# Kernel tuning notes

Hardware: AMD Instinct MI355X
Metric: run time of the kernel (lower is better)

## Reference

```python
import jax, jax.numpy as jnp
import numpy as np

B, D, H, W = 16, 384, 64, 64
Dq, Dv, NH, DFF = 768, 384, 12, 1536
EPS = 1e-5


def setup_inputs() -> dict:
    key = jax.random.key(0)
    ks = jax.random.split(key, 8)

    def w(k, out_c, in_c):
        return (jax.random.normal(k, (out_c, in_c), jnp.float32) / np.float32(np.sqrt(in_c)))

    return {
        "x": jax.random.normal(ks[0], (B, D, H, W), jnp.float32),
        "ln1_w": jnp.ones((D, H, W), jnp.float32),
        "ln1_b": jnp.zeros((D, H, W), jnp.float32),
        "qw": w(ks[1], Dq, D), "qb": jnp.zeros((Dq,), jnp.float32),
        "kw": w(ks[2], Dq, D), "kb": jnp.zeros((Dq,), jnp.float32),
        "vw": w(ks[3], Dv, D), "vb": jnp.zeros((Dv,), jnp.float32),
        "hu_w": w(ks[4], D, Dv), "hu_b": jnp.zeros((D,), jnp.float32),
        "ln2_w": jnp.ones((D, H, W), jnp.float32),
        "ln2_b": jnp.zeros((D, H, W), jnp.float32),
        "ff1_w": w(ks[5], DFF, D), "ff1_b": jnp.zeros((DFF,), jnp.float32),
        "ff2_w": w(ks[6], D, DFF), "ff2_b": jnp.zeros((D,), jnp.float32),
    }


def layernorm(x, w, b):
    # torch.nn.LayerNorm((D, H, W)): normalize over last 3 dims, biased var
    mu = x.mean(axis=(1, 2, 3), keepdims=True)
    var = x.var(axis=(1, 2, 3), keepdims=True)
    return (x - mu) * jax.lax.rsqrt(var + EPS) * w + b


def conv1x1(x, w, b):
    # 1x1 conv == channel-mixing matmul; x: (B, Cin, H, W), w: (Cout, Cin)
    return jnp.einsum('bdhw,od->bohw', x, w) + b[None, :, None, None]


def reference(x, ln1_w, ln1_b, qw, qb, kw, kb, vw, vb, hu_w, hu_b,
              ln2_w, ln2_b, ff1_w, ff1_b, ff2_w, ff2_b):
    a = layernorm(x, ln1_w, ln1_b)
    Q = conv1x1(a, qw, qb)  # (B, Dq, H, W)
    K = conv1x1(a, kw, kb)  # (B, Dq, H, W)
    V = conv1x1(a, vw, vb)  # (B, Dv, H, W)

    Q = jax.nn.softmax(Q, axis=1)  # softmax over channels (subtract-max is built in)
    K = jax.nn.softmax(K.reshape(B, Dq, H * W), axis=-1).reshape(B, Dq, H, W)

    Qh = Q.reshape(B, NH, Dq // NH, H, W)
    Kh = K.reshape(B, NH, Dq // NH, H, W)
    Vh = V.reshape(B, NH, Dv // NH, H, W)

    # kernel_size=1: adaptive_avg_pool2d(KV, 1) * 1 == spatial mean of K (x) V,
    # and the grouped 1x1 conv is a per-(batch,head) (Dv/h x Dq/h) matmul on Q.
    KV = jnp.einsum('bhqyx,bhvyx->bhqv', Kh, Vh) / np.float32(H * W)
    QKV = jnp.einsum('bhqv,bhqyx->bhvyx', KV, Qh).reshape(B, Dv, H, W)

    attn = conv1x1(QKV, hu_w, hu_b)  # head unification, (B, D, H, W)
    x = x + attn
    x = layernorm(x, ln2_w, ln2_b)
    ff = conv1x1(jax.nn.gelu(conv1x1(x, ff1_w, ff1_b), approximate=False), ff2_w, ff2_b)
    return x + ff
```

## Files before the change

kernel.cpp:

```cpp
#include <hip/hip_runtime.h>
#include <hip/hip_bf16.h>

using u16 = unsigned short;
typedef __attribute__((ext_vector_type(4))) float f32x4;
typedef __bf16 bf16x8 __attribute__((ext_vector_type(8)));
typedef short s16x4 __attribute__((ext_vector_type(4)));
typedef short s16x8 __attribute__((ext_vector_type(8)));

#define DEVI __device__ __forceinline__

DEVI float b2f(u16 u) {
    union { unsigned i; float f; } x; x.i = ((unsigned)u) << 16; return x.f;
}
DEVI u16 f2b(float f) {
    union { float f; unsigned i; } x; x.f = f;
    unsigned r = (x.i + 0x7fffu + ((x.i >> 16) & 1u)) >> 16;
    return (u16)r;
}

DEVI float gelu_fast(float v) {
    float t = v * (1.5957691f + 0.0713548162f * v * v);
    return v / (1.f + __expf(-t));
}

static constexpr long long PX = 1572864LL;
static constexpr long long PQ = 3145728LL;
static constexpr long long PH = 6291456LL;

DEVI void gl_lds16(const u16* g, u16* l) {
    __builtin_amdgcn_global_load_lds(
        (const __attribute__((address_space(1))) unsigned int*)g,
        (__attribute__((address_space(3))) unsigned int*)l, 16, 0, 0);
}

__global__ __launch_bounds__(256)
void wconv_kernel(const float* __restrict__ qw, const float* __restrict__ kw,
                  const float* __restrict__ vw, const float* __restrict__ huw,
                  const float* __restrict__ ff1w, const float* __restrict__ ff2w,
                  u16* __restrict__ wcv)
{
    int blk = blockIdx.x;
    const float* src; u16* dst; int lb;
    if      (blk < 288)  { src = qw;   dst = wcv;           lb = blk; }
    else if (blk < 576)  { src = kw;   dst = wcv + 294912;  lb = blk - 288; }
    else if (blk < 720)  { src = vw;   dst = wcv + 589824;  lb = blk - 576; }
    else if (blk < 864)  { src = huw;  dst = wcv + 737280;  lb = blk - 720; }
    else if (blk < 1440) { src = ff1w; dst = wcv + 884736;  lb = blk - 864; }
    else                 { src = ff2w; dst = wcv + 1474560; lb = blk - 1440; }
    int i = (lb * 256 + threadIdx.x) * 4;
    f32x4 v = *(const f32x4*)(src + i);
    s16x4 o;
#pragma unroll
    for (int j = 0; j < 4; ++j) o[j] = (short)f2b(v[j]);
    *(s16x4*)(dst + i) = o;
}

__global__ __launch_bounds__(256)
void bcat_kernel(const float* __restrict__ qb, const float* __restrict__ kb,
                 const float* __restrict__ vb, float* __restrict__ o)
{
    int i = blockIdx.x * 256 + threadIdx.x;
    if (i < 768)       o[i] = qb[i];
    else if (i < 1536) o[i] = kb[i - 768];
    else if (i < 1920) o[i] = vb[i - 1536];
}

__global__ __launch_bounds__(256, 4)
void gemm_qkv_kernel(const u16* __restrict__ A, long long strideA,
                     const u16* __restrict__ Bw,
                     const float* __restrict__ bias,
                     u16* __restrict__ Q, u16* __restrict__ Kd, u16* __restrict__ V,
                     int K)
{
    const int tid = threadIdx.x;
    const int lane = tid & 63;
    const int wv = tid >> 6;
    const int wr = wv >> 1, wc = wv & 1;
    const int l15 = lane & 15, l4 = lane >> 4;
    const int bm = blockIdx.x, bn = blockIdx.y, bz = blockIdx.z;

    A += (long long)bz * strideA;
    u16* dstBase; int Nout; int colBase;
    if (bn < 6)       { dstBase = Q  + (long long)bz * PQ; Nout = 768; colBase = bn * 128; }
    else if (bn < 12) { dstBase = Kd + (long long)bz * PQ; Nout = 768; colBase = (bn - 6) * 128; }
    else              { dstBase = V  + (long long)bz * PX; Nout = 384; colBase = (bn - 12) * 128; }

    __shared__ u16 lds[2][128 * 64];

    f32x4 acc[4][4] = {};

    auto stage = [&](int kt) {
#pragma unroll
        for (int i = 0; i < 4; ++i) {
            int cid = tid + i * 256;
            int row = cid >> 3, c8 = cid & 7;
            int c8s = c8 ^ (row & 7);
            gl_lds16(A + (long long)(bm * 128 + row) * K + kt + c8s * 8,
                     &lds[0][cid * 8]);
        }
#pragma unroll
        for (int i = 0; i < 4; ++i) {
            int cid = tid + i * 256;
            int row = cid >> 3, c8 = cid & 7;
            int c8s = c8 ^ (row & 7);
            gl_lds16(Bw + (long long)(bn * 128 + row) * K + kt + c8s * 8,
                     &lds[1][cid * 8]);
        }
    };

    auto compute = [&]() {
#pragma unroll
        for (int kk = 0; kk < 2; ++kk) {
            bf16x8 af[4], bfr[4];
#pragma unroll
            for (int mi = 0; mi < 4; ++mi) {
                int row = wr * 64 + mi * 16 + l15;
                int idx8 = (kk * 4 + l4) ^ (row & 7);
                af[mi] = *(const bf16x8*)&lds[0][row * 64 + idx8 * 8];
            }
#pragma unroll
            for (int ni = 0; ni < 4; ++ni) {
                int row = wc * 64 + ni * 16 + l15;
                int idx8 = (kk * 4 + l4) ^ (row & 7);
                bfr[ni] = *(const bf16x8*)&lds[1][row * 64 + idx8 * 8];
            }
#pragma unroll
            for (int mi = 0; mi < 4; ++mi)
#pragma unroll
                for (int ni = 0; ni < 4; ++ni)
                    acc[mi][ni] = __builtin_amdgcn_mfma_f32_16x16x32_bf16(af[mi], bfr[ni], acc[mi][ni], 0, 0, 0);
        }
    };

    stage(0);
    asm volatile("s_waitcnt vmcnt(0)" ::: "memory");
    __syncthreads();
    for (int kt = 64; kt < K; kt += 64) {
        compute();
        __syncthreads();
        stage(kt);
        asm volatile("s_waitcnt vmcnt(0)" ::: "memory");
        __syncthreads();
    }
    compute();

    u16* st = &lds[0][0];
#pragma unroll
    for (int p = 0; p < 2; ++p) {
        __syncthreads();
        if (wr == p) {
#pragma unroll
            for (int ni = 0; ni < 4; ++ni) {
                int colL = wc * 64 + ni * 16 + l15;
                float bv = bias[bn * 128 + colL];
#pragma unroll
                for (int mi = 0; mi < 4; ++mi) {
#pragma unroll
                    for (int r = 0; r < 4; ++r)
                        st[(mi * 16 + l4 * 4 + r) * 136 + colL] = f2b(acc[mi][ni][r] + bv);
                }
            }
        }
        __syncthreads();
        int lr = tid >> 2, q = tid & 3;
        const u16* src = st + lr * 136 + q * 32;
        u16* dst = dstBase + (long long)(bm * 128 + p * 64 + lr) * Nout + colBase + q * 32;
#pragma unroll
        for (int j = 0; j < 4; ++j)
            *(s16x8*)(dst + j * 8) = *(const s16x8*)(src + j * 8);
    }
}

__global__ __launch_bounds__(256, 4)
void gemm_attn_kernel(const u16* __restrict__ A, long long strideA,
                      const u16* __restrict__ Bw, long long strideB,
                      const float* __restrict__ bias,
                      const float* __restrict__ x,
                      u16* __restrict__ sT,
                      float* __restrict__ part2, int K)
{
    const int tid = threadIdx.x;
    const int lane = tid & 63;
    const int wv = tid >> 6;
    const int wr = wv >> 1, wc = wv & 1;
    const int l15 = lane & 15, l4 = lane >> 4;
    const int bm = blockIdx.x, bn = blockIdx.y, bz = blockIdx.z;

    A  += (long long)bz * strideA;
    Bw += (long long)bz * strideB;
    x  += (long long)bz * PX;
    sT += (long long)bz * PX;

    __shared__ u16 lds[2][128 * 64];

    f32x4 acc[4][4] = {};

    auto stage = [&](int kt) {
#pragma unroll
        for (int i = 0; i < 4; ++i) {
            int cid = tid + i * 256;
            int row = cid >> 3, c8 = cid & 7;
            int c8s = c8 ^ (row & 7);
            gl_lds16(A + (long long)(bm * 128 + row) * K + kt + c8s * 8,
                     &lds[0][cid * 8]);
        }
#pragma unroll
        for (int i = 0; i < 4; ++i) {
            int cid = tid + i * 256;
            int row = cid >> 3, c8 = cid & 7;
            int c8s = c8 ^ (row & 7);
            gl_lds16(Bw + (long long)(bn * 128 + row) * K + kt + c8s * 8,
                     &lds[1][cid * 8]);
        }
    };

    auto compute = [&]() {
#pragma unroll
        for (int kk = 0; kk < 2; ++kk) {
            bf16x8 af[4], bfr[4];
#pragma unroll
            for (int mi = 0; mi < 4; ++mi) {
                int row = wr * 64 + mi * 16 + l15;
                int idx8 = (kk * 4 + l4) ^ (row & 7);
                af[mi] = *(const bf16x8*)&lds[0][row * 64 + idx8 * 8];
            }
#pragma unroll
            for (int ni = 0; ni < 4; ++ni) {
                int row = wc * 64 + ni * 16 + l15;
                int idx8 = (kk * 4 + l4) ^ (row & 7);
                bfr[ni] = *(const bf16x8*)&lds[1][row * 64 + idx8 * 8];
            }
#pragma unroll
            for (int mi = 0; mi < 4; ++mi)
#pragma unroll
                for (int ni = 0; ni < 4; ++ni)
                    acc[mi][ni] = __builtin_amdgcn_mfma_f32_16x16x32_bf16(af[mi], bfr[ni], acc[mi][ni], 0, 0, 0);
        }
    };

    stage(0);
    asm volatile("s_waitcnt vmcnt(0)" ::: "memory");
    __syncthreads();
    for (int kt = 64; kt < K; kt += 64) {
        compute();
        __syncthreads();
        stage(kt);
        asm volatile("s_waitcnt vmcnt(0)" ::: "memory");
        __syncthreads();
    }
    compute();

    u16* st = &lds[0][0];
    float ps = 0.f, pq = 0.f;
#pragma unroll
    for (int p = 0; p < 2; ++p) {
        __syncthreads();
        if (wr == p) {
#pragma unroll
            for (int ni = 0; ni < 4; ++ni) {
                int colL = wc * 64 + ni * 16 + l15;
                int colG = bn * 128 + colL;
                float bv = bias[colG];
#pragma unroll
                for (int mi = 0; mi < 4; ++mi) {
                    const float* xp = x + (long long)colG * 4096 + bm * 128 + p * 64 + mi * 16 + l4 * 4;
                    f32x4 xv = *(const f32x4*)xp;
#pragma unroll
                    for (int r = 0; r < 4; ++r)
                        st[(mi * 16 + l4 * 4 + r) * 136 + colL] = f2b(acc[mi][ni][r] + bv + xv[r]);
                }
            }
        }
        __syncthreads();
        int lr = tid >> 2, q = tid & 3;
        const u16* src = st + lr * 136 + q * 32;
        u16* dst = sT + (long long)(bm * 128 + p * 64 + lr) * 384 + bn * 128 + q * 32;
#pragma unroll
        for (int j = 0; j < 4; ++j) {
            s16x8 v = *(const s16x8*)(src + j * 8);
            *(s16x8*)(dst + j * 8) = v;
#pragma unroll
            for (int e = 0; e < 8; ++e) { float f = b2f((u16)v[e]); ps += f; pq += f * f; }
        }
    }

    for (int off = 32; off; off >>= 1) { ps += __shfl_down(ps, off); pq += __shfl_down(pq, off); }
    __shared__ float rs[4], rq[4];
    if (lane == 0) { rs[wv] = ps; rq[wv] = pq; }
    __syncthreads();
    if (tid == 0) {
        int bid = bz * 96 + bm * 3 + bn;
        part2[bid * 2 + 0] = rs[0] + rs[1] + rs[2] + rs[3];
        part2[bid * 2 + 1] = rq[0] + rq[1] + rq[2] + rq[3];
    }
}

__global__ __launch_bounds__(256, 4)
void gemm_bt_kernel(const u16* __restrict__ A, long long strideA,
                    const u16* __restrict__ Bw, long long strideB,
                    const float* __restrict__ bias,
                    u16* __restrict__ C, long long strideC,
                    float* __restrict__ Cf,
                    const u16* __restrict__ addT, long long strideAdd,
                    int K, int N, int doGelu)
{
    const int tid = threadIdx.x;
    const int lane = tid & 63;
    const int wv = tid >> 6;
    const int wr = wv >> 1, wc = wv & 1;
    const int l15 = lane & 15, l4 = lane >> 4;
    const int bm = blockIdx.x, bn = blockIdx.y, bz = blockIdx.z;

    A  += (long long)bz * strideA;
    Bw += (long long)bz * strideB;
    if (C)    C    += (long long)bz * strideC;
    if (Cf)   Cf   += (long long)bz * strideC;
    if (addT) addT += (long long)bz * strideAdd;

    __shared__ u16 lds[2][128 * 64];

    f32x4 acc[4][4] = {};

    auto stage = [&](int kt) {
#pragma unroll
        for (int i = 0; i < 4; ++i) {
            int cid = tid + i * 256;
            int row = cid >> 3, c8 = cid & 7;
            int c8s = c8 ^ (row & 7);
            gl_lds16(A + (long long)(bm * 128 + row) * K + kt + c8s * 8,
                     &lds[0][cid * 8]);
        }
#pragma unroll
        for (int i = 0; i < 4; ++i) {
            int cid = tid + i * 256;
            int row = cid >> 3, c8 = cid & 7;
            int c8s = c8 ^ (row & 7);
            gl_lds16(Bw + (long long)(bn * 128 + row) * K + kt + c8s * 8,
                     &lds[1][cid * 8]);
        }
    };

    auto compute = [&]() {
#pragma unroll
        for (int kk = 0; kk < 2; ++kk) {
            bf16x8 af[4], bfr[4];
#pragma unroll
            for (int mi = 0; mi < 4; ++mi) {
                int row = wr * 64 + mi * 16 + l15;
                int idx8 = (kk * 4 + l4) ^ (row & 7);
                af[mi] = *(const bf16x8*)&lds[0][row * 64 + idx8 * 8];
            }
#pragma unroll
            for (int ni = 0; ni < 4; ++ni) {
                int row = wc * 64 + ni * 16 + l15;
                int idx8 = (kk * 4 + l4) ^ (row & 7);
                bfr[ni] = *(const bf16x8*)&lds[1][row * 64 + idx8 * 8];
            }
#pragma unroll
            for (int mi = 0; mi < 4; ++mi)
#pragma unroll
                for (int ni = 0; ni < 4; ++ni)
                    acc[mi][ni] = __builtin_amdgcn_mfma_f32_16x16x32_bf16(af[mi], bfr[ni], acc[mi][ni], 0, 0, 0);
        }
    };

    stage(0);
    asm volatile("s_waitcnt vmcnt(0)" ::: "memory");
    __syncthreads();
    for (int kt = 64; kt < K; kt += 64) {
        compute();
        __syncthreads();
        stage(kt);
        asm volatile("s_waitcnt vmcnt(0)" ::: "memory");
        __syncthreads();
    }
    compute();

    if (!Cf) {
        u16* st = &lds[0][0];
#pragma unroll
        for (int p = 0; p < 2; ++p) {
            __syncthreads();
            if (wr == p) {
#pragma unroll
                for (int ni = 0; ni < 4; ++ni) {
                    int colL = wc * 64 + ni * 16 + l15;
                    float bv = bias ? bias[bn * 128 + colL] : 0.f;
#pragma unroll
                    for (int mi = 0; mi < 4; ++mi) {
#pragma unroll
                        for (int r = 0; r < 4; ++r) {
                            float v = acc[mi][ni][r] + bv;
                            if (doGelu) v = gelu_fast(v);
                            st[(mi * 16 + l4 * 4 + r) * 136 + colL] = f2b(v);
                        }
                    }
                }
            }
            __syncthreads();
            int lr = tid >> 2, q = tid & 3;
            const u16* src = st + lr * 136 + q * 32;
            u16* dst = C + (long long)(bm * 128 + p * 64 + lr) * N + bn * 128 + q * 32;
#pragma unroll
            for (int j = 0; j < 4; ++j)
                *(s16x8*)(dst + j * 8) = *(const s16x8*)(src + j * 8);
        }
    } else {
        float* stf = (float*)&lds[0][0];
#pragma unroll
        for (int p = 0; p < 4; ++p) {
            __syncthreads();
            if (wc == (p >> 1)) {
#pragma unroll
                for (int nj = 0; nj < 2; ++nj) {
                    int ni = (p & 1) * 2 + nj;
                    int colL = wc * 64 + ni * 16 + l15;
                    int lc = nj * 16 + l15;
                    float bv = bias ? bias[bn * 128 + colL] : 0.f;
#pragma unroll
                    for (int mi = 0; mi < 4; ++mi) {
                        int row0 = wr * 64 + mi * 16 + l4 * 4;
#pragma unroll
                        for (int r = 0; r < 4; ++r) {
                            float v = acc[mi][ni][r] + bv
                                    + b2f(addT[(long long)(bm * 128 + row0 + r) * N + bn * 128 + colL]);
                            stf[lc * 132 + row0 + r] = v;
                        }
                    }
                }
            }
            __syncthreads();
            int lc = tid >> 3, q = tid & 7;
            float* dst = Cf + (long long)(bn * 128 + p * 32 + lc) * 4096 + bm * 128 + q * 16;
            const float* src = stf + lc * 132 + q * 16;
#pragma unroll
            for (int j = 0; j < 4; ++j)
                *(f32x4*)(dst + j * 4) = *(const f32x4*)(src + j * 4);
        }
    }
}

__global__ __launch_bounds__(256)
void stats_part_kernel(const float* __restrict__ x, float* __restrict__ part)
{
    int b = blockIdx.x, cb = blockIdx.y, t = threadIdx.x;
    const float* p = x + (long long)b * PX + (long long)cb * 49152;
    float s = 0.f, q = 0.f;
    for (int i = 0; i < 48; ++i) {
        f32x4 v = *(const f32x4*)(p + (i * 256 + t) * 4);
#pragma unroll
        for (int j = 0; j < 4; ++j) { s += v[j]; q += v[j] * v[j]; }
    }
    for (int off = 32; off; off >>= 1) { s += __shfl_down(s, off); q += __shfl_down(q, off); }
    __shared__ float rs[4], rq[4];
    if ((t & 63) == 0) { rs[t >> 6] = s; rq[t >> 6] = q; }
    __syncthreads();
    if (t == 0) {
        part[(b * 32 + cb) * 2 + 0] = rs[0] + rs[1] + rs[2] + rs[3];
        part[(b * 32 + cb) * 2 + 1] = rq[0] + rq[1] + rq[2] + rq[3];
    }
}

__global__ void stats_fin_kernel(const float* __restrict__ part, float* __restrict__ mu, float* __restrict__ rsg)
{
    int b = blockIdx.x, l = threadIdx.x;
    float s = l < 32 ? part[(b * 32 + l) * 2 + 0] : 0.f;
    float q = l < 32 ? part[(b * 32 + l) * 2 + 1] : 0.f;
    for (int off = 32; off; off >>= 1) { s += __shfl_down(s, off); q += __shfl_down(q, off); }
    if (l == 0) {
        float m = s / 1572864.f;
        float v = q / 1572864.f - m * m; v = fmaxf(v, 0.f);
        mu[b] = m; rsg[b] = rsqrtf(v + 1e-5f);
    }
}

__global__ __launch_bounds__(256)
void ln_apply_T_kernel(const float* __restrict__ src, const float* __restrict__ w, const float* __restrict__ bb,
                       const float* __restrict__ mu, const float* __restrict__ rsg, u16* __restrict__ dstT)
{
    int nt = blockIdx.x, dt = blockIdx.y, b = blockIdx.z;
    int t = threadIdx.x, tx = t & 63, ty = t >> 6;
    __shared__ float tile[64][65];
    float m = mu[b], r = rsg[b];
    const long long base = (long long)b * PX;
#pragma unroll 4
    for (int i = 0; i < 16; ++i) {
        int dy = ty + i * 4;
        int d = dt * 64 + dy, n = nt * 64 + tx;
        long long widx = (long long)d * 4096 + n;
        tile[dy][tx] = (src[base + widx] - m) * r * w[widx] + bb[widx];
    }
    __syncthreads();
#pragma unroll 4
    for (int i = 0; i < 16; ++i) {
        int ny = ty + i * 4;
        int n = nt * 64 + ny, d = dt * 64 + tx;
        dstT[base + (long long)n * 384 + d] = f2b(tile[tx][ny]);
    }
}

__global__ __launch_bounds__(256)
void softmax_rows_kernel(u16* __restrict__ QT)
{
    long long row = (long long)blockIdx.x * 4 + (threadIdx.x >> 6);
    int lane = threadIdx.x & 63;
    u16* p = QT + row * 768;
    float v[12];
#pragma unroll
    for (int g = 0; g < 3; ++g) {
        s16x4 a = *(const s16x4*)(p + g * 256 + lane * 4);
#pragma unroll
        for (int j = 0; j < 4; ++j) v[g * 4 + j] = b2f((u16)a[j]);
    }
    float m = -1e30f;
#pragma unroll
    for (int j = 0; j < 12; ++j) m = fmaxf(m, v[j]);
    for (int off = 32; off; off >>= 1) m = fmaxf(m, __shfl_xor(m, off));
    float s = 0.f;
#pragma unroll
    for (int j = 0; j < 12; ++j) { v[j] = __expf(v[j] - m); s += v[j]; }
    for (int off = 32; off; off >>= 1) s += __shfl_xor(s, off);
    float inv = 1.f / s;
#pragma unroll
    for (int g = 0; g < 3; ++g) {
        s16x4 o;
#pragma unroll
        for (int j = 0; j < 4; ++j) o[j] = (short)f2b(v[g * 4 + j] * inv);
        *(s16x4*)(p + g * 256 + lane * 4) = o;
    }
}

__global__ __launch_bounds__(256)
void kv_part_kernel(const u16* __restrict__ KT, const u16* __restrict__ VT,
                    u16* __restrict__ KVp, float* __restrict__ sp)
{
    const int ch = blockIdx.x, h = blockIdx.y, b = blockIdx.z;
    const int t = threadIdx.x;
    const int lane = t & 63, w = t >> 6;

    __shared__ u16 kraw[128 * 64];
    __shared__ u16 eKT[64 * 128];
    __shared__ u16 Vt[32 * 128];
    __shared__ float reds[4][64];

    const u16* Kp = KT + (long long)b * PQ + (long long)(ch * 128) * 768 + h * 64;
    const u16* Vp = VT + (long long)b * PX + (long long)(ch * 128) * 384 + h * 32;

#pragma unroll
    for (int pass = 0; pass < 4; ++pass) {
        int cid = t + pass * 256;
        int row = cid >> 3, c8 = cid & 7;
        gl_lds16(Kp + (long long)row * 768 + c8 * 8, kraw + cid * 8);
    }

    {
        int v0 = (t & 7) * 4;
#pragma unroll
        for (int pass = 0; pass < 4; ++pass) {
            int n = (t >> 3) + pass * 32;
            s16x4 v4 = *(const s16x4*)(Vp + (long long)n * 384 + v0);
#pragma unroll
            for (int j = 0; j < 4; ++j) {
                int row = v0 + j;
                Vt[row * 128 + (n ^ ((row & 7) << 3))] = (u16)v4[j];
            }
        }
    }

    asm volatile("s_waitcnt vmcnt(0)" ::: "memory");
    __syncthreads();

    const int c = lane;
    {
        float s = 0.f;
        const int swz = (c & 7) << 3;
#pragma unroll
        for (int r8 = 0; r8 < 4; ++r8) {
            int rbase = w * 32 + r8 * 8;
            s16x8 buf;
#pragma unroll
            for (int j = 0; j < 8; ++j) {
                float e = __expf(b2f(kraw[(rbase + j) * 64 + c]));
                s += e;
                buf[j] = (short)f2b(e);
            }
            *(s16x8*)&eKT[c * 128 + (rbase ^ swz)] = buf;
        }
        reds[w][c] = s;
    }
    __syncthreads();

    if (t < 64)
        sp[((long long)(b * 12 + h) * 32 + ch) * 64 + t] =
            reds[0][t] + reds[1][t] + reds[2][t] + reds[3][t];

    const int l15 = lane & 15, l4 = lane >> 4;
    const int qrow = w * 16 + l15;
    const int sa = (qrow & 7) << 3;
    const int v0row = l15, v1row = 16 + l15;
    const int s0 = (v0row & 7) << 3, s1 = (v1row & 7) << 3;
    f32x4 acc0 = {}, acc1 = {};
#pragma unroll
    for (int ns = 0; ns < 4; ++ns) {
        int na = ns * 32 + l4 * 8;
        bf16x8 a  = *(const bf16x8*)&eKT[qrow * 128 + (na ^ sa)];
        bf16x8 b0 = *(const bf16x8*)&Vt[v0row * 128 + (na ^ s0)];
        bf16x8 b1 = *(const bf16x8*)&Vt[v1row * 128 + (na ^ s1)];
        acc0 = __builtin_amdgcn_mfma_f32_16x16x32_bf16(a, b0, acc0, 0, 0, 0);
        acc1 = __builtin_amdgcn_mfma_f32_16x16x32_bf16(a, b1, acc1, 0, 0, 0);
    }
    u16* Kb = KVp + ((long long)(b * 12 + h) * 32 + ch) * 2048;
#pragma unroll
    for (int r = 0; r < 4; ++r) {
        int q = w * 16 + l4 * 4 + r;
        Kb[q * 32 + l15]      = f2b(acc0[r]);
        Kb[q * 32 + 16 + l15] = f2b(acc1[r]);
    }
}

__global__ __launch_bounds__(256)
void kv_fin_kernel(const u16* __restrict__ KVp, const float* __restrict__ sp,
                   u16* __restrict__ WeffT)
{
    const int h = blockIdx.x, b = blockIdx.y;
    const int t = threadIdx.x;
    __shared__ float fac[64];
    __shared__ float kvt[32][64];

    const long long pb = (long long)(b * 12 + h) * 32;
    if (t < 64) {
        float s = 0.f;
#pragma unroll
        for (int ch = 0; ch < 32; ++ch) s += sp[(pb + ch) * 64 + t];
        fac[t] = 1.f / (s * 4096.f);
    }
    __syncthreads();

    const int v0 = (t & 3) * 8, q = t >> 2;
    float acc[8] = {};
#pragma unroll
    for (int ch = 0; ch < 32; ++ch) {
        s16x8 kv8 = *(const s16x8*)&KVp[(pb + ch) * 2048 + q * 32 + v0];
#pragma unroll
        for (int j = 0; j < 8; ++j) acc[j] += b2f((u16)kv8[j]);
    }
    float fq = fac[q];
#pragma unroll
    for (int j = 0; j < 8; ++j) kvt[v0 + j][q] = acc[j] * fq;
    __syncthreads();

    u16* Wb = WeffT + (long long)b * 294912;
    for (int i = t; i < 64 * 384; i += 256) {
        int qq = i / 384, cc = i % 384;
        int cv = cc - h * 32;
        float val = (cv >= 0 && cv < 32) ? kvt[cv][qq] : 0.f;
        Wb[(long long)(h * 64 + qq) * 384 + cc] = f2b(val);
    }
}

__global__ __launch_bounds__(256)
void wtrans_kernel(const float* __restrict__ w, const float* __restrict__ bb,
                   u16* __restrict__ wT, u16* __restrict__ bT)
{
    int nt = blockIdx.x, dt = blockIdx.y;
    const float* src = blockIdx.z ? bb : w;
    u16* dst = blockIdx.z ? bT : wT;
    int t = threadIdx.x, tx = t & 63, ty = t >> 6;
    __shared__ float tile[64][65];
#pragma unroll 4
    for (int i = 0; i < 16; ++i) {
        int dy = ty + i * 4;
        tile[dy][tx] = src[(long long)(dt * 64 + dy) * 4096 + nt * 64 + tx];
    }
    __syncthreads();
#pragma unroll 4
    for (int i = 0; i < 16; ++i) {
        int ny = ty + i * 4;
        dst[(long long)(nt * 64 + ny) * 384 + dt * 64 + tx] = f2b(tile[tx][ny]);
    }
}

__global__ __launch_bounds__(256)
void stats_fin2_kernel(const float* __restrict__ part2, float* __restrict__ mu, float* __restrict__ rsg)
{
    int b = blockIdx.x, t = threadIdx.x;
    float s = 0.f, q = 0.f;
    if (t < 96) { s = part2[(b * 96 + t) * 2]; q = part2[(b * 96 + t) * 2 + 1]; }
    for (int off = 32; off; off >>= 1) { s += __shfl_down(s, off); q += __shfl_down(q, off); }
    __shared__ float rs[4], rq[4];
    if ((t & 63) == 0) { rs[t >> 6] = s; rq[t >> 6] = q; }
    __syncthreads();
    if (t == 0) {
        float S = rs[0] + rs[1] + rs[2] + rs[3], Q = rq[0] + rq[1] + rq[2] + rq[3];
        float m = S / 1572864.f;
        float v = Q / 1572864.f - m * m; v = fmaxf(v, 0.f);
        mu[b] = m; rsg[b] = rsqrtf(v + 1e-5f);
    }
}

__global__ __launch_bounds__(256)
void ln2_apply_kernel(const u16* __restrict__ sT, const u16* __restrict__ wT, const u16* __restrict__ bT,
                      const float* __restrict__ mu, const float* __restrict__ rsg, u16* __restrict__ x2T)
{
    int blk = blockIdx.x, b = blockIdx.y, t = threadIdx.x;
    float m = mu[b], r = rsg[b];
    long long wi = (long long)blk * 2048 + t * 8;
    long long gi = (long long)b * PX + wi;
    s16x8 sv = *(const s16x8*)(sT + gi);
    s16x8 wv = *(const s16x8*)(wT + wi);
    s16x8 bv = *(const s16x8*)(bT + wi);
    s16x8 o;
#pragma unroll
    for (int j = 0; j < 8; ++j)
        o[j] = (short)f2b((b2f((u16)sv[j]) - m) * r * b2f((u16)wv[j]) + b2f((u16)bv[j]));
    *(s16x8*)(x2T + gi) = o;
}

extern "C" void kernel_launch(void* const* d_in, const int* in_sizes, int n_in,
                              void* d_out, int out_size, void* d_ws, size_t ws_size,
                              hipStream_t stream)
{
    const float* x    = (const float*)d_in[0];
    const float* ln1w = (const float*)d_in[1];
    const float* ln1b = (const float*)d_in[2];
    const float* qw   = (const float*)d_in[3];
    const float* qb   = (const float*)d_in[4];
    const float* kw   = (const float*)d_in[5];
    const float* kb   = (const float*)d_in[6];
    const float* vw   = (const float*)d_in[7];
    const float* vb   = (const float*)d_in[8];
    const float* huw  = (const float*)d_in[9];
    const float* hub  = (const float*)d_in[10];
    const float* ln2w = (const float*)d_in[11];
    const float* ln2b = (const float*)d_in[12];
    const float* ff1w = (const float*)d_in[13];
    const float* ff1b = (const float*)d_in[14];
    const float* ff2w = (const float*)d_in[15];
    const float* ff2b = (const float*)d_in[16];
    float* out = (float*)d_out;

    char* ws = (char*)d_ws;
    u16*   aT    = (u16*)(ws + 0);
    u16*   QT    = (u16*)(ws + 50331648LL);
    u16*   KT    = (u16*)(ws + 150994944LL);
    u16*   VT    = (u16*)(ws + 251658240LL);
    u16*   WeffT = (u16*)(ws + 301989888LL);
    u16*   wcv   = (u16*)(ws + 311427072LL);
    float* fbuf  = (float*)(ws + 315555840LL);

    u16*   KVp    = (u16*)(ws + 0);
    float* sp     = (float*)(ws + 25165824LL);
    u16*   WcombB = (u16*)(ws + 27525120LL);

    u16* sT = KT;
    u16* wT = (u16*)(ws + 150994944LL + 50331648LL);
    u16* bT = (u16*)(ws + 150994944LL + 53477376LL);
    u16* g8 = KT;

    u16* x2T = QT;

    u16* qwB   = wcv;
    u16* ff1wB = wcv + 884736;
    u16* ff2wB = wcv + 1474560;
    u16* huwB  = wcv + 737280;

    float* part1 = fbuf;
    float* mu1   = fbuf + 1024;
    float* rs1   = fbuf + 1040;
    float* part2 = fbuf + 1056;
    float* mu2   = part2 + 3072;
    float* rs2   = mu2 + 16;
    float* qkvb  = rs2 + 16;

    wconv_kernel<<<2016, 256, 0, stream>>>(qw, kw, vw, huw, ff1w, ff2w, wcv);
    bcat_kernel<<<8, 256, 0, stream>>>(qb, kb, vb, qkvb);

    stats_part_kernel<<<dim3(16, 32), 256, 0, stream>>>(x, part1);
    stats_fin_kernel<<<16, 64, 0, stream>>>(part1, mu1, rs1);
    ln_apply_T_kernel<<<dim3(64, 6, 16), 256, 0, stream>>>(x, ln1w, ln1b, mu1, rs1, aT);

    gemm_qkv_kernel<<<dim3(32, 15, 16), 256, 0, stream>>>(aT, PX, qwB, qkvb, QT, KT, VT, 384);

    softmax_rows_kernel<<<16384, 256, 0, stream>>>(QT);

    kv_part_kernel<<<dim3(32, 12, 16), 256, 0, stream>>>(KT, VT, KVp, sp);
    kv_fin_kernel<<<dim3(12, 16), 256, 0, stream>>>(KVp, sp, WeffT);

    wtrans_kernel<<<dim3(64, 6, 2), 256, 0, stream>>>(ln2w, ln2b, wT, bT);

    gemm_bt_kernel<<<dim3(3, 6, 16), 256, 0, stream>>>(huwB, 0, WeffT, 294912, nullptr, WcombB, 294912, nullptr, nullptr, 0, 384, 768, 0);

    gemm_attn_kernel<<<dim3(32, 3, 16), 256, 0, stream>>>(QT, PQ, WcombB, 294912, hub, x, sT, part2, 768);

    stats_fin2_kernel<<<16, 256, 0, stream>>>(part2, mu2, rs2);
    ln2_apply_kernel<<<dim3(768, 16), 256, 0, stream>>>(sT, wT, bT, mu2, rs2, x2T);

    for (int c = 0; c < 2; ++c) {
        gemm_bt_kernel<<<dim3(32, 12, 8), 256, 0, stream>>>(
            x2T + (long long)c * 8 * PX, PX, ff1wB, 0, ff1b,
            g8, PH, nullptr, nullptr, 0, 384, 1536, 1);
        gemm_bt_kernel<<<dim3(32, 3, 8), 256, 0, stream>>>(
            g8, PH, ff2wB, 0, ff2b,
            nullptr, PX, out + (long long)c * 8 * PX,
            x2T + (long long)c * 8 * PX, PX, 1536, 384, 0);
    }
}
```

Baseline: 735.4 us.

## Fold Q softmax into QKV GEMM epilogue and fuse head-unify weight build

```diff
diff --git a/kernel.cpp b/kernel.cpp
--- a/kernel.cpp
+++ b/kernel.cpp
@@ -70,7 +70,7 @@
                      const u16* __restrict__ Bw,
                      const float* __restrict__ bias,
                      u16* __restrict__ Q, u16* __restrict__ Kd, u16* __restrict__ V,
-                     int K)
+                     float* __restrict__ rsump, int K)
 {
     const int tid = threadIdx.x;
     const int lane = tid & 63;
@@ -84,6 +84,7 @@
     if (bn < 6)       { dstBase = Q  + (long long)bz * PQ; Nout = 768; colBase = bn * 128; }
     else if (bn < 12) { dstBase = Kd + (long long)bz * PQ; Nout = 768; colBase = (bn - 6) * 128; }
     else              { dstBase = V  + (long long)bz * PX; Nout = 384; colBase = (bn - 12) * 128; }
+    const bool isQ = (bn < 6);
 
     __shared__ u16 lds[2][128 * 64];
 
@@ -156,8 +157,11 @@
 #pragma unroll
                 for (int mi = 0; mi < 4; ++mi) {
 #pragma unroll
-                    for (int r = 0; r < 4; ++r)
-                        st[(mi * 16 + l4 * 4 + r) * 136 + colL] = f2b(acc[mi][ni][r] + bv);
+                    for (int r = 0; r < 4; ++r) {
+                        float v = acc[mi][ni][r] + bv;
+                        if (isQ) v = __expf(v);
+                        st[(mi * 16 + l4 * 4 + r) * 136 + colL] = f2b(v);
+                    }
                 }
             }
         }
@@ -165,9 +169,22 @@
         int lr = tid >> 2, q = tid & 3;
         const u16* src = st + lr * 136 + q * 32;
         u16* dst = dstBase + (long long)(bm * 128 + p * 64 + lr) * Nout + colBase + q * 32;
-#pragma unroll
-        for (int j = 0; j < 4; ++j)
-            *(s16x8*)(dst + j * 8) = *(const s16x8*)(src + j * 8);
+        float s = 0.f;
+#pragma unroll
+        for (int j = 0; j < 4; ++j) {
+            s16x8 v8 = *(const s16x8*)(src + j * 8);
+            *(s16x8*)(dst + j * 8) = v8;
+            if (isQ) {
+#pragma unroll
+                for (int e = 0; e < 8; ++e) s += b2f((u16)v8[e]);
+            }
+        }
+        if (isQ) {
+            s += __shfl_xor(s, 1);
+            s += __shfl_xor(s, 2);
+            if (q == 0)
+                rsump[((long long)(bz * 6 + bn)) * 4096 + bm * 128 + p * 64 + lr] = s;
+        }
     }
 }
 
@@ -176,6 +193,7 @@
                       const u16* __restrict__ Bw, long long strideB,
                       const float* __restrict__ bias,
                       const float* __restrict__ x,
+                      const float* __restrict__ rsump,
                       u16* __restrict__ sT,
                       float* __restrict__ part2, int K)
 {
@@ -192,6 +210,15 @@
     sT += (long long)bz * PX;
 
     __shared__ u16 lds[2][128 * 64];
+    __shared__ float sscale[128];
+
+    if (tid < 128) {
+        float s = 0.f;
+#pragma unroll
+        for (int j = 0; j < 6; ++j)
+            s += rsump[((long long)(bz * 6 + j)) * 4096 + bm * 128 + tid];
+        sscale[tid] = 1.f / s;
+    }
 
     f32x4 acc[4][4] = {};
 
@@ -266,8 +293,10 @@
                     const float* xp = x + (long long)colG * 4096 + bm * 128 + p * 64 + mi * 16 + l4 * 4;
                     f32x4 xv = *(const f32x4*)xp;
 #pragma unroll
-                    for (int r = 0; r < 4; ++r)
-                        st[(mi * 16 + l4 * 4 + r) * 136 + colL] = f2b(acc[mi][ni][r] + bv + xv[r]);
+                    for (int r = 0; r < 4; ++r) {
+                        float ss = sscale[p * 64 + mi * 16 + l4 * 4 + r];
+                        st[(mi * 16 + l4 * 4 + r) * 136 + colL] = f2b(acc[mi][ni][r] * ss + bv + xv[r]);
+                    }
                 }
             }
         }
@@ -500,37 +529,6 @@
 }
 
 __global__ __launch_bounds__(256)
-void softmax_rows_kernel(u16* __restrict__ QT)
-{
-    long long row = (long long)blockIdx.x * 4 + (threadIdx.x >> 6);
-    int lane = threadIdx.x & 63;
-    u16* p = QT + row * 768;
-    float v[12];
-#pragma unroll
-    for (int g = 0; g < 3; ++g) {
-        s16x4 a = *(const s16x4*)(p + g * 256 + lane * 4);
-#pragma unroll
-        for (int j = 0; j < 4; ++j) v[g * 4 + j] = b2f((u16)a[j]);
-    }
-    float m = -1e30f;
-#pragma unroll
-    for (int j = 0; j < 12; ++j) m = fmaxf(m, v[j]);
-    for (int off = 32; off; off >>= 1) m = fmaxf(m, __shfl_xor(m, off));
-    float s = 0.f;
-#pragma unroll
-    for (int j = 0; j < 12; ++j) { v[j] = __expf(v[j] - m); s += v[j]; }
-    for (int off = 32; off; off >>= 1) s += __shfl_xor(s, off);
-    float inv = 1.f / s;
-#pragma unroll
-    for (int g = 0; g < 3; ++g) {
-        s16x4 o;
-#pragma unroll
-        for (int j = 0; j < 4; ++j) o[j] = (short)f2b(v[g * 4 + j] * inv);
-        *(s16x4*)(p + g * 256 + lane * 4) = o;
-    }
-}
-
-__global__ __launch_bounds__(256)
 void kv_part_kernel(const u16* __restrict__ KT, const u16* __restrict__ VT,
                     u16* __restrict__ KVp, float* __restrict__ sp)
 {
@@ -620,12 +618,22 @@
 
 __global__ __launch_bounds__(256)
 void kv_fin_kernel(const u16* __restrict__ KVp, const float* __restrict__ sp,
-                   u16* __restrict__ WeffT)
+                   const u16* __restrict__ huwB, u16* __restrict__ Wcomb)
 {
     const int h = blockIdx.x, b = blockIdx.y;
     const int t = threadIdx.x;
+    const int lane = t & 63, w = t >> 6;
+    const int l15 = lane & 15, l4 = lane >> 4;
+
     __shared__ float fac[64];
-    __shared__ float kvt[32][64];
+    __shared__ u16 kvq[64 * 40];
+    __shared__ u16 hw[384 * 40];
+
+    for (int i = t; i < 384 * 4; i += 256) {
+        int row = i >> 2, seg = i & 3;
+        *(s16x8*)&hw[row * 40 + seg * 8] =
+            *(const s16x8*)(huwB + row * 384 + h * 32 + seg * 8);
+    }
 
     const long long pb = (long long)(b * 12 + h) * 32;
     if (t < 64) {
@@ -636,25 +644,49 @@
     }
     __syncthreads();
 
-    const int v0 = (t & 3) * 8, q = t >> 2;
-    float acc[8] = {};
-#pragma unroll
-    for (int ch = 0; ch < 32; ++ch) {
-        s16x8 kv8 = *(const s16x8*)&KVp[(pb + ch) * 2048 + q * 32 + v0];
-#pragma unroll
-        for (int j = 0; j < 8; ++j) acc[j] += b2f((u16)kv8[j]);
-    }
-    float fq = fac[q];
-#pragma unroll
-    for (int j = 0; j < 8; ++j) kvt[v0 + j][q] = acc[j] * fq;
-    __syncthreads();
-
-    u16* Wb = WeffT + (long long)b * 294912;
-    for (int i = t; i < 64 * 384; i += 256) {
-        int qq = i / 384, cc = i % 384;
-        int cv = cc - h * 32;
-        float val = (cv >= 0 && cv < 32) ? kvt[cv][qq] : 0.f;
-        Wb[(long long)(h * 64 + qq) * 384 + cc] = f2b(val);
+    {
+        const int v0 = (t & 3) * 8, q = t >> 2;
+        float acc[8] = {};
+#pragma unroll
+        for (int ch = 0; ch < 32; ++ch) {
+            s16x8 kv8 = *(const s16x8*)&KVp[(pb + ch) * 2048 + q * 32 + v0];
+#pragma unroll
+            for (int j = 0; j < 8; ++j) acc[j] += b2f((u16)kv8[j]);
+        }
+        float fq = fac[q];
+        s16x8 o;
+#pragma unroll
+        for (int j = 0; j < 8; ++j) o[j] = (short)f2b(acc[j] * fq);
+        *(s16x8*)&kvq[q * 40 + v0] = o;
+    }
+    __syncthreads();
+
+    bf16x8 af[6], bfr[4];
+#pragma unroll
+    for (int mi = 0; mi < 6; ++mi)
+        af[mi] = *(const bf16x8*)&hw[(w * 96 + mi * 16 + l15) * 40 + l4 * 8];
+#pragma unroll
+    for (int ni = 0; ni < 4; ++ni)
+        bfr[ni] = *(const bf16x8*)&kvq[(ni * 16 + l15) * 40 + l4 * 8];
+    f32x4 acc[6][4] = {};
+#pragma unroll
+    for (int mi = 0; mi < 6; ++mi)
+#pragma unroll
+        for (int ni = 0; ni < 4; ++ni)
+            acc[mi][ni] = __builtin_amdgcn_mfma_f32_16x16x32_bf16(af[mi], bfr[ni], acc[mi][ni], 0, 0, 0);
+
+    u16* Wb = Wcomb + (long long)b * 294912;
+#pragma unroll
+    for (int mi = 0; mi < 6; ++mi) {
+#pragma unroll
+        for (int ni = 0; ni < 4; ++ni) {
+            int col = h * 64 + ni * 16 + l15;
+#pragma unroll
+            for (int r = 0; r < 4; ++r) {
+                int o = w * 96 + mi * 16 + l4 * 4 + r;
+                Wb[o * 768 + col] = f2b(acc[mi][ni][r]);
+            }
+        }
     }
 }
 
@@ -744,7 +776,7 @@
     u16*   QT    = (u16*)(ws + 50331648LL);
     u16*   KT    = (u16*)(ws + 150994944LL);
     u16*   VT    = (u16*)(ws + 251658240LL);
-    u16*   WeffT = (u16*)(ws + 301989888LL);
+    float* rsump = (float*)(ws + 301989888LL);
     u16*   wcv   = (u16*)(ws + 311427072LL);
     float* fbuf  = (float*)(ws + 315555840LL);
 
@@ -779,18 +811,15 @@
     stats_fin_kernel<<<16, 64, 0, stream>>>(part1, mu1, rs1);
     ln_apply_T_kernel<<<dim3(64, 6, 16), 256, 0, stream>>>(x, ln1w, ln1b, mu1, rs1, aT);
 
-    gemm_qkv_kernel<<<dim3(32, 15, 16), 256, 0, stream>>>(aT, PX, qwB, qkvb, QT, KT, VT, 384);
-
-    softmax_rows_kernel<<<16384, 256, 0, stream>>>(QT);
+    gemm_qkv_kernel<<<dim3(32, 15, 16), 256, 0, stream>>>(aT, PX, qwB, qkvb, QT, KT, VT, rsump, 384);
 
     kv_part_kernel<<<dim3(32, 12, 16), 256, 0, stream>>>(KT, VT, KVp, sp);
-    kv_fin_kernel<<<dim3(12, 16), 256, 0, stream>>>(KVp, sp, WeffT);
+
+    kv_fin_kernel<<<dim3(12, 16), 256, 0, stream>>>(KVp, sp, huwB, WcombB);
 
     wtrans_kernel<<<dim3(64, 6, 2), 256, 0, stream>>>(ln2w, ln2b, wT, bT);
 
-    gemm_bt_kernel<<<dim3(3, 6, 16), 256, 0, stream>>>(huwB, 0, WeffT, 294912, nullptr, WcombB, 294912, nullptr, nullptr, 0, 384, 768, 0);
-
-    gemm_attn_kernel<<<dim3(32, 3, 16), 256, 0, stream>>>(QT, PQ, WcombB, 294912, hub, x, sT, part2, 768);
+    gemm_attn_kernel<<<dim3(32, 3, 16), 256, 0, stream>>>(QT, PQ, WcombB, 294912, hub, x, rsump, sT, part2, 768);
 
     stats_fin2_kernel<<<16, 256, 0, stream>>>(part2, mu2, rs2);
     ln2_apply_kernel<<<dim3(768, 16), 256, 0, stream>>>(sT, wT, bT, mu2, rs2, x2T);
```

New measurement: 693.5 us. -5.7%, faster.
